# Optimization experiments

Hardware: AMD Instinct MI355X
Metric: run time of the kernel (lower is better)

Reference implementation:

```python
import jax, jax.numpy as jnp
import numpy as np

N = 50000   # nodes
E = 800000  # edges (avg degree 16)
IN = 128    # in_dim
R = 4       # rank
CMB = 64    # combine_dim
H = 4       # heads
D = 64      # hidden_dim per head
NEG_SLOPE = 0.2


def setup_inputs() -> dict:
    key = jax.random.key(0)
    ks = iter(jax.random.split(key, 24))
    def rnd(shape, s):
        return jax.random.normal(next(ks), shape, jnp.float32) * s
    src = jax.random.randint(next(ks), (E,), 0, N, jnp.int32)
    dst = jax.random.randint(next(ks), (E,), 0, N, jnp.int32)
    ones = jnp.ones((N, 1), jnp.float32)
    # buffers built in __init__: features with a trailing ones column
    h_common = jnp.concatenate([rnd((N, IN), 1.0), ones], axis=-1)      # (N, 129)
    h_type = jnp.concatenate([rnd((N, 512), 1.0), ones], axis=-1)       # (N, 513)
    h_rel = jnp.concatenate([rnd((N, 512), 1.0), ones], axis=-1)        # (N, 513)
    return {
        'src': src, 'dst': dst,
        'h_common': h_common, 'h_type': h_type, 'h_rel': h_rel,
        'Wc': rnd((R, IN + 1, CMB), 0.05),
        'Wt': rnd((R, 513, CMB), 0.05),
        'Wr': rnd((R, 513, CMB), 0.05),
        'fw': rnd((1, R), 0.5),
        'fb': rnd((1, CMB), 0.1),
        'W0': rnd((CMB, H * D), 0.05),
        'al0': rnd((H, D), 0.05), 'ar0': rnd((H, D), 0.05),
        'b0': rnd((H * D,), 0.05),
        'W1': rnd((H * D, H * D), 0.05),
        'al1': rnd((H, D), 0.05), 'ar1': rnd((H, D), 0.05),
        'b1': rnd((H * D,), 0.05),
    }


def _gat_layer(h, src, dst, W, al, ar, b, residual):
    # h: (N, F_in) -> out: (N, H*D), attention a: (E, H)
    feat = (h @ W).reshape(N, H, D)
    el = jnp.einsum('nhd,hd->nh', feat, al)  # (N, H)
    er = jnp.einsum('nhd,hd->nh', feat, ar)
    e = jax.nn.leaky_relu(el[src] + er[dst], NEG_SLOPE)  # (E, H)
    # edge softmax over incoming edges of each dst node
    m = jax.ops.segment_max(e, dst, num_segments=N)      # (N, H)
    ee = jnp.exp(e - m[dst])
    s = jax.ops.segment_sum(ee, dst, num_segments=N)
    a = ee / s[dst]                                       # (E, H)
    msg = feat[src] * a[:, :, None]                       # (E, H, D)
    out = jax.ops.segment_sum(msg, dst, num_segments=N)   # (N, H, D)
    if residual:
        out = out + h.reshape(N, H, D)
    out = out + b.reshape(1, H, D)
    return out.reshape(N, H * D), a


def reference(src, dst, h_common, h_type, h_rel, Wc, Wt, Wr, fw, fb,
              W0, al0, ar0, b0, W1, al1, ar1, b1):
    # low-rank trilinear fusion
    fc = jnp.einsum('ni,ric->rnc', h_common, Wc)  # (R, N, CMB)
    ft = jnp.einsum('ni,ric->rnc', h_type, Wt)
    fr = jnp.einsum('ni,ric->rnc', h_rel, Wr)
    zy = fc * ft * fr
    h = jnp.einsum('r,rnc->nc', fw[0], zy) + fb   # (N, CMB)
    h = jax.nn.elu(h)
    # stacked GAT layers
    h, att = _gat_layer(h, src, dst, W0, al0, ar0, b0, residual=False)
    h, att = _gat_layer(h, src, dst, W1, al1, ar1, b1, residual=True)
    return h, att
```

## Files before the change

### kernel.cpp

```cpp
#include <hip/hip_runtime.h>
#include <math.h>

#define NN 50000
#define EE 800000
#define NEG 0.2f
#define NG (NN / 16)

using f32x4  = __attribute__((ext_vector_type(4))) float;
using bf16x8 = __attribute__((ext_vector_type(8))) short;

__device__ __forceinline__ float lrelu(float x){ return x > 0.f ? x : NEG*x; }

__device__ __forceinline__ unsigned short f2b(float f){
    unsigned int u = __float_as_uint(f);
    return (unsigned short)((u + 0x7FFFu + ((u >> 16) & 1u)) >> 16);
}
__device__ __forceinline__ float b2f(unsigned short h){
    return __uint_as_float(((unsigned int)h) << 16);
}
__device__ __forceinline__ void gld_lds16(const void* g, void* l){
    __builtin_amdgcn_global_load_lds(
        (const __attribute__((address_space(1))) unsigned int*)g,
        (__attribute__((address_space(3))) unsigned int*)l, 16, 0, 0);
}

__global__ void pack_w_fusion(const float* __restrict__ W, unsigned short* __restrict__ out,
                              int K, int NKC)
{
    int u = blockIdx.x * blockDim.x + threadIdx.x;
    if (u >= NKC * 16 * 64) return;
    int l = u & 63, chunk = (u >> 6) & 15, kc = u >> 10;
    int ct = chunk >> 2, r = chunk & 3;
    int c = ct * 16 + (l & 15);
    int kb = kc * 32 + (l >> 4) * 8;
    bf16x8 v;
#pragma unroll
    for (int j = 0; j < 8; ++j)
        v[j] = (short)f2b(W[((size_t)r * K + kb + j) * 64 + c]);
    *(bf16x8*)(out + (size_t)u * 8) = v;
}

template<int PERM>
__global__ void pack_w_gemm(const float* __restrict__ W, unsigned short* __restrict__ out,
                            int K, int C)
{
    int NCH = C / 16;
    int total = (K / 32) * NCH * 64;
    int u = blockIdx.x * blockDim.x + threadIdx.x;
    if (u >= total) return;
    int l = u & 63, ch = (u >> 6) % NCH, kc = u / (64 * NCH);
    int c = ch * 16 + (l & 15);
    int kb = kc * 32 + (l >> 4) * 8;
    bf16x8 v;
#pragma unroll
    for (int j = 0; j < 8; ++j) {
        int k = kb + j;
        int ko = PERM ? ((k & 3) * 64 + (k >> 2)) : k;
        v[j] = (short)f2b(W[(size_t)ko * C + c]);
    }
    *(bf16x8*)(out + (size_t)u * 8) = v;
}

template<int KT, int NKC>
__global__ __launch_bounds__(256) void pack_a_tile(
    const float* __restrict__ F, unsigned short* __restrict__ out)
{
    constexpr int TILES = NKC / 4;
    __shared__ float sf[16][130];
    const int tid = threadIdx.x;
    const int g = blockIdx.x / TILES, t = blockIdx.x % TILES;
    const int nb = g * 16, k0 = t * 128;

#pragma unroll
    for (int i = 0; i < 8; ++i) {
        int idx = tid + i * 256;
        int row = idx >> 7, k = idx & 127;
        sf[row][k] = F[(size_t)(nb + row) * KT + k0 + k];
    }
    __syncthreads();
    {
        int kcl = tid >> 6, l = tid & 63;
        int row = l & 15, kb = kcl * 32 + (l >> 4) * 8;
        bf16x8 o;
#pragma unroll
        for (int j = 0; j < 8; ++j) o[j] = (short)f2b(sf[row][kb + j]);
        *(bf16x8*)(out + ((size_t)(g * NKC + t * 4 + kcl) * 64 + l) * 8) = o;
    }
}

template<int NKC>
__device__ __forceinline__ void fusion_pass_lds(
    const unsigned short* __restrict__ ldsA, int cbase,
    const unsigned short* __restrict__ wp,
    const float* __restrict__ W, int K, int w, int l, f32x4 (&acc)[4])
{
    const int c_lo = l & 15;
#pragma unroll
    for (int ct = 0; ct < 4; ++ct) {
        float wi = W[((size_t)w * K + (K - 1)) * 64 + ct * 16 + c_lo];
        acc[ct] = f32x4{wi, wi, wi, wi};
    }
#pragma unroll
    for (int kc = 0; kc < NKC; ++kc) {
        bf16x8 af = *(const bf16x8*)(ldsA + (cbase + kc) * 512 + l * 8);
        const unsigned short* wk = wp + (size_t)kc * 8192 + w * 512 + l * 8;
#pragma unroll
        for (int ct = 0; ct < 4; ++ct) {
            bf16x8 bf = *(const bf16x8*)(wk + ct * 2048);
            acc[ct] = __builtin_amdgcn_mfma_f32_16x16x32_bf16(af, bf, acc[ct], 0, 0, 0);
        }
    }
}

__global__ __launch_bounds__(256) void fusion_mfma(
    const unsigned short* __restrict__ apc, const unsigned short* __restrict__ apt,
    const unsigned short* __restrict__ apr,
    const unsigned short* __restrict__ wpc, const unsigned short* __restrict__ wpt,
    const unsigned short* __restrict__ wpr,
    const float* __restrict__ Wc, const float* __restrict__ Wt, const float* __restrict__ Wr,
    const float* __restrict__ fw, const float* __restrict__ fb,
    unsigned short* __restrict__ h0b)
{
    __shared__ __align__(16) char smem[36864];
    unsigned short* ldsA = (unsigned short*)smem;
    float* ldsx = (float*)smem;
    const int w = threadIdx.x >> 6, l = threadIdx.x & 63;
    const int G = blockIdx.x;

#pragma unroll
    for (int j = 0; j < 9; ++j) {
        int cid = w * 9 + j;
        const unsigned short* s;
        if (cid < 4)       s = apc + ((size_t)G * 4  + cid) * 512;
        else if (cid < 20) s = apt + ((size_t)G * 16 + (cid - 4)) * 512;
        else               s = apr + ((size_t)G * 16 + (cid - 20)) * 512;
        gld_lds16(s + l * 8, ldsA + cid * 512);
    }
    __syncthreads();

    f32x4 prod[4], acc[4];
    fusion_pass_lds<4>(ldsA, 0, wpc, Wc, 129, w, l, acc);
#pragma unroll
    for (int ct = 0; ct < 4; ++ct) prod[ct] = acc[ct];
    fusion_pass_lds<16>(ldsA, 4, wpt, Wt, 513, w, l, acc);
#pragma unroll
    for (int ct = 0; ct < 4; ++ct) prod[ct] *= acc[ct];
    fusion_pass_lds<16>(ldsA, 20, wpr, Wr, 513, w, l, acc);
    const float fww = fw[w];
#pragma unroll
    for (int ct = 0; ct < 4; ++ct) prod[ct] = prod[ct] * acc[ct] * fww;

    __syncthreads();
#pragma unroll
    for (int ct = 0; ct < 4; ++ct)
        *(f32x4*)&ldsx[((w * 4 + ct) * 64 + l) * 4] = prod[ct];
    __syncthreads();

    f32x4 s = *(const f32x4*)&ldsx[((0 * 4 + w) * 64 + l) * 4];
#pragma unroll
    for (int r = 1; r < 4; ++r)
        s += *(const f32x4*)&ldsx[((r * 4 + w) * 64 + l) * 4];

    const int c = w * 16 + (l & 15);
    const float fbc = fb[c];
#pragma unroll
    for (int q = 0; q < 4; ++q) {
        int n = G * 16 + (l >> 4) * 4 + q;
        float v = s[q] + fbc;
        v = v > 0.f ? v : expm1f(v);
        h0b[(size_t)n * 64 + c] = f2b(v);
    }
}

template<int K>
__global__ __launch_bounds__(256) void gemm_reg(
    const unsigned short* __restrict__ Ab, const unsigned short* __restrict__ wp,
    const float* __restrict__ al, const float* __restrict__ ar,
    unsigned short* __restrict__ featb,
    float* __restrict__ el, float* __restrict__ er)
{
    constexpr int NKC = K / 32;
    const int w = threadIdx.x >> 6, l = threadIdx.x & 63;
    const int nb = blockIdx.x * 16;

    f32x4 acc[4];
#pragma unroll
    for (int i = 0; i < 4; ++i) acc[i] = f32x4{0.f, 0.f, 0.f, 0.f};

    const unsigned short* abase = Ab + (size_t)(nb + (l & 15)) * K + (l >> 4) * 8;
    bf16x8 afs[NKC];
#pragma unroll
    for (int kc = 0; kc < NKC; ++kc)
        afs[kc] = *(const bf16x8*)(abase + kc * 32);

    bf16x8 bcur[4];
    {
        const unsigned short* wk = wp + (size_t)(0 * 16 + w * 4) * 512 + l * 8;
#pragma unroll
        for (int i = 0; i < 4; ++i) bcur[i] = *(const bf16x8*)(wk + i * 512);
    }
#pragma unroll
    for (int kc = 0; kc < NKC; ++kc) {
        bf16x8 bnxt[4];
        if (kc + 1 < NKC) {
            const unsigned short* wk = wp + ((size_t)(kc + 1) * 16 + w * 4) * 512 + l * 8;
#pragma unroll
            for (int i = 0; i < 4; ++i) bnxt[i] = *(const bf16x8*)(wk + i * 512);
        }
#pragma unroll
        for (int i = 0; i < 4; ++i)
            acc[i] = __builtin_amdgcn_mfma_f32_16x16x32_bf16(afs[kc], bcur[i], acc[i], 0, 0, 0);
        if (kc + 1 < NKC) {
#pragma unroll
            for (int i = 0; i < 4; ++i) bcur[i] = bnxt[i];
        }
    }

#pragma unroll
    for (int i = 0; i < 4; ++i) {
        int c = (w * 4 + i) * 16 + (l & 15);
        int dm = (c & 63) * 4 + (c >> 6);
#pragma unroll
        for (int q = 0; q < 4; ++q) {
            int n = nb + (l >> 4) * 4 + q;
            featb[(size_t)n * 256 + dm] = f2b(acc[i][q]);
        }
    }

    float pel[4] = {0.f, 0.f, 0.f, 0.f};
    float per_[4] = {0.f, 0.f, 0.f, 0.f};
#pragma unroll
    for (int i = 0; i < 4; ++i) {
        int d = i * 16 + (l & 15);
        float av = al[w * 64 + d];
        float rv = ar[w * 64 + d];
#pragma unroll
        for (int q = 0; q < 4; ++q) {
            pel[q] += acc[i][q] * av;
            per_[q] += acc[i][q] * rv;
        }
    }
#pragma unroll
    for (int off = 1; off <= 8; off <<= 1) {
#pragma unroll
        for (int q = 0; q < 4; ++q) {
            pel[q] += __shfl_xor(pel[q], off);
            per_[q] += __shfl_xor(per_[q], off);
        }
    }
    int qsel = l & 15;
    if (qsel < 4) {
        float ev = qsel == 0 ? pel[0] : qsel == 1 ? pel[1] : qsel == 2 ? pel[2] : pel[3];
        float rv = qsel == 0 ? per_[0] : qsel == 1 ? per_[1] : qsel == 2 ? per_[2] : per_[3];
        int n = nb + (l >> 4) * 4 + qsel;
        el[(size_t)n * 4 + w] = ev;
        er[(size_t)n * 4 + w] = rv;
    }
}

__global__ void hist_kernel(const int* __restrict__ dst, int* __restrict__ cnt)
{
    int e = blockIdx.x * blockDim.x + threadIdx.x;
    if (e < EE) atomicAdd(&cnt[dst[e]], 1);
}

__global__ __launch_bounds__(1024) void scan_kernel(const int* __restrict__ cnt, int* __restrict__ offs)
{
    __shared__ int tmp[1024];
    const int t = threadIdx.x;
    const int C = (NN + 1023) / 1024;
    int lo = t * C, hi = min(lo + C, NN);
    int s = 0;
    for (int i = lo; i < hi; ++i) s += cnt[i];
    tmp[t] = s;
    __syncthreads();
    for (int off = 1; off < 1024; off <<= 1) {
        int v = (t >= off) ? tmp[t - off] : 0;
        __syncthreads();
        tmp[t] += v;
        __syncthreads();
    }
    int run = (t == 0) ? 0 : tmp[t - 1];
    for (int i = lo; i < hi; ++i) { offs[i] = run; run += cnt[i]; }
    if (t == 1023) offs[NN] = tmp[1023];
}

__global__ void scatter_kernel(const int* __restrict__ dst, const int* __restrict__ offs,
                               int* __restrict__ cur, int* __restrict__ esort)
{
    int e = blockIdx.x * blockDim.x + threadIdx.x;
    if (e < EE) {
        int d = dst[e];
        int p = offs[d] + atomicAdd(&cur[d], 1);
        esort[p] = e;
    }
}

template <int RESID, int WATT, int WB16, int WF32>
__global__ __launch_bounds__(256) void gat_agg(
    const int* __restrict__ esort, const int* __restrict__ src, const int* __restrict__ offs,
    const unsigned short* __restrict__ featb,
    const float* __restrict__ el, const float* __restrict__ er,
    const unsigned short* __restrict__ residb, const float* __restrict__ bias,
    float* __restrict__ out, unsigned short* __restrict__ outb,
    float4* __restrict__ att)
{
    int n = (int)((blockIdx.x * (size_t)blockDim.x + threadIdx.x) >> 6);
    int lane = threadIdx.x & 63;
    if (n >= NN) return;
    const int s0 = offs[n], s1 = offs[n + 1], deg = s1 - s0;
    const float4 r4 = *(const float4*)(er + (size_t)n * 4);

    float a0 = 0.f, a1 = 0.f, a2 = 0.f, a3 = 0.f;
    float i0, i1, i2, i3;

    if (deg <= 64) {
        int p = s0 + lane;
        bool valid = p < s1;
        int e = valid ? esort[p] : 0;
        int sv = valid ? src[e] : 0;
        float v0 = -1e30f, v1 = -1e30f, v2 = -1e30f, v3 = -1e30f;
        if (valid) {
            float4 l4 = *(const float4*)(el + (size_t)sv * 4);
            v0 = lrelu(l4.x + r4.x); v1 = lrelu(l4.y + r4.y);
            v2 = lrelu(l4.z + r4.z); v3 = lrelu(l4.w + r4.w);
        }
        float m0 = v0, m1 = v1, m2 = v2, m3 = v3;
#pragma unroll
        for (int off = 32; off; off >>= 1) {
            m0 = fmaxf(m0, __shfl_xor(m0, off));
            m1 = fmaxf(m1, __shfl_xor(m1, off));
            m2 = fmaxf(m2, __shfl_xor(m2, off));
            m3 = fmaxf(m3, __shfl_xor(m3, off));
        }
        float e0 = valid ? expf(v0 - m0) : 0.f;
        float e1 = valid ? expf(v1 - m1) : 0.f;
        float e2 = valid ? expf(v2 - m2) : 0.f;
        float e3 = valid ? expf(v3 - m3) : 0.f;
        float z0 = e0, z1 = e1, z2 = e2, z3 = e3;
#pragma unroll
        for (int off = 32; off; off >>= 1) {
            z0 += __shfl_xor(z0, off);
            z1 += __shfl_xor(z1, off);
            z2 += __shfl_xor(z2, off);
            z3 += __shfl_xor(z3, off);
        }
        float j0 = z0 > 0.f ? 1.f / z0 : 0.f;
        float j1 = z1 > 0.f ? 1.f / z1 : 0.f;
        float j2 = z2 > 0.f ? 1.f / z2 : 0.f;
        float j3 = z3 > 0.f ? 1.f / z3 : 0.f;
        e0 *= j0; e1 *= j1; e2 *= j2; e3 *= j3;
        if (WATT && valid)
            att[e] = make_float4(e0, e1, e2, e3);
        for (int jj = 0; jj < deg; ++jj) {
            float w0 = __shfl(e0, jj), w1 = __shfl(e1, jj);
            float w2 = __shfl(e2, jj), w3 = __shfl(e3, jj);
            int s = __shfl(sv, jj);
            ushort4 f = *(const ushort4*)(featb + (size_t)s * 256 + lane * 4);
            a0 += w0 * b2f(f.x);
            a1 += w1 * b2f(f.y);
            a2 += w2 * b2f(f.z);
            a3 += w3 * b2f(f.w);
        }
        i0 = i1 = i2 = i3 = 1.f;
    } else {
        float m0 = -1e30f, m1 = -1e30f, m2 = -1e30f, m3 = -1e30f;
        for (int p = s0 + lane; p < s1; p += 64) {
            int s = src[esort[p]];
            float4 l4 = *(const float4*)(el + (size_t)s * 4);
            m0 = fmaxf(m0, lrelu(l4.x + r4.x));
            m1 = fmaxf(m1, lrelu(l4.y + r4.y));
            m2 = fmaxf(m2, lrelu(l4.z + r4.z));
            m3 = fmaxf(m3, lrelu(l4.w + r4.w));
        }
#pragma unroll
        for (int off = 32; off; off >>= 1) {
            m0 = fmaxf(m0, __shfl_xor(m0, off));
            m1 = fmaxf(m1, __shfl_xor(m1, off));
            m2 = fmaxf(m2, __shfl_xor(m2, off));
            m3 = fmaxf(m3, __shfl_xor(m3, off));
        }
        float z0 = 0.f, z1 = 0.f, z2 = 0.f, z3 = 0.f;
        for (int p = s0 + lane; p < s1; p += 64) {
            int s = src[esort[p]];
            float4 l4 = *(const float4*)(el + (size_t)s * 4);
            z0 += expf(lrelu(l4.x + r4.x) - m0);
            z1 += expf(lrelu(l4.y + r4.y) - m1);
            z2 += expf(lrelu(l4.z + r4.z) - m2);
            z3 += expf(lrelu(l4.w + r4.w) - m3);
        }
#pragma unroll
        for (int off = 32; off; off >>= 1) {
            z0 += __shfl_xor(z0, off);
            z1 += __shfl_xor(z1, off);
            z2 += __shfl_xor(z2, off);
            z3 += __shfl_xor(z3, off);
        }
        i0 = z0 > 0.f ? 1.f / z0 : 0.f;
        i1 = z1 > 0.f ? 1.f / z1 : 0.f;
        i2 = z2 > 0.f ? 1.f / z2 : 0.f;
        i3 = z3 > 0.f ? 1.f / z3 : 0.f;
        for (int p = s0; p < s1; ++p) {
            int e = esort[p];
            int s = src[e];
            float4 l4 = *(const float4*)(el + (size_t)s * 4);
            float w0 = expf(lrelu(l4.x + r4.x) - m0);
            float w1 = expf(lrelu(l4.y + r4.y) - m1);
            float w2 = expf(lrelu(l4.z + r4.z) - m2);
            float w3 = expf(lrelu(l4.w + r4.w) - m3);
            ushort4 f = *(const ushort4*)(featb + (size_t)s * 256 + lane * 4);
            a0 += w0 * b2f(f.x);
            a1 += w1 * b2f(f.y);
            a2 += w2 * b2f(f.z);
            a3 += w3 * b2f(f.w);
            if (WATT && lane == 0)
                att[e] = make_float4(w0 * i0, w1 * i1, w2 * i2, w3 * i3);
        }
    }

    float o0 = a0 * i0 + bias[lane];
    float o1 = a1 * i1 + bias[64 + lane];
    float o2 = a2 * i2 + bias[128 + lane];
    float o3 = a3 * i3 + bias[192 + lane];
    if (RESID) {
        ushort4 rp = *(const ushort4*)(residb + (size_t)n * 256 + lane * 4);
        o0 += b2f(rp.x); o1 += b2f(rp.y); o2 += b2f(rp.z); o3 += b2f(rp.w);
    }
    if (WF32) {
        float* op = out + (size_t)n * 256;
        op[lane] = o0;
        op[64 + lane] = o1;
        op[128 + lane] = o2;
        op[192 + lane] = o3;
    }
    if (WB16) {
        ushort4 ob;
        ob.x = f2b(o0); ob.y = f2b(o1); ob.z = f2b(o2); ob.w = f2b(o3);
        *(ushort4*)(outb + (size_t)n * 256 + lane * 4) = ob;
    }
}

extern "C" void kernel_launch(void* const* d_in, const int* in_sizes, int n_in,
                              void* d_out, int out_size, void* d_ws, size_t ws_size,
                              hipStream_t stream)
{
    const int*   src = (const int*)d_in[0];
    const int*   dst = (const int*)d_in[1];
    const float* hc  = (const float*)d_in[2];
    const float* ht  = (const float*)d_in[3];
    const float* hr  = (const float*)d_in[4];
    const float* Wc  = (const float*)d_in[5];
    const float* Wt  = (const float*)d_in[6];
    const float* Wr  = (const float*)d_in[7];
    const float* fw  = (const float*)d_in[8];
    const float* fb  = (const float*)d_in[9];
    const float* W0  = (const float*)d_in[10];
    const float* al0 = (const float*)d_in[11];
    const float* ar0 = (const float*)d_in[12];
    const float* b0  = (const float*)d_in[13];
    const float* W1  = (const float*)d_in[14];
    const float* al1 = (const float*)d_in[15];
    const float* ar1 = (const float*)d_in[16];
    const float* b1  = (const float*)d_in[17];

    char* ws = (char*)d_ws;
    unsigned short* h0b   = (unsigned short*)(ws);
    unsigned short* h1b   = (unsigned short*)(ws + 6400000);
    unsigned short* featb = (unsigned short*)(ws + 32000000);
    float* el    = (float*)(ws + 57600000);
    float* er    = (float*)(ws + 58400000);
    int*   cnt   = (int*)  (ws + 59200000);
    int*   offs  = (int*)  (ws + 59400000);
    int*   esort = (int*)  (ws + 59600128);
    unsigned short* wpc = (unsigned short*)(ws + 62800128);
    unsigned short* wpt = (unsigned short*)(ws + 62865664);
    unsigned short* wpr = (unsigned short*)(ws + 63127808);
    unsigned short* wp0 = (unsigned short*)(ws + 63389952);
    unsigned short* wp1 = (unsigned short*)(ws + 63422720);
    if (ws_size < 63553792ull) return;

    float* outh = (float*)d_out;
    float4* atto = (float4*)(outh + (size_t)NN * 256);

    unsigned short* apt = (unsigned short*)d_out;
    unsigned short* apc = (unsigned short*)((char*)d_out + 51200000);
    unsigned short* apr = (unsigned short*)(ws + 6400000);

    pack_w_fusion<<<(4 * 16 * 64 + 255) / 256, 256, 0, stream>>>(Wc, wpc, 129, 4);
    pack_w_fusion<<<(16 * 16 * 64 + 255) / 256, 256, 0, stream>>>(Wt, wpt, 513, 16);
    pack_w_fusion<<<(16 * 16 * 64 + 255) / 256, 256, 0, stream>>>(Wr, wpr, 513, 16);
    pack_w_gemm<0><<<(2 * 16 * 64 + 255) / 256, 256, 0, stream>>>(W0, wp0, 64, 256);
    pack_w_gemm<1><<<(8 * 16 * 64 + 255) / 256, 256, 0, stream>>>(W1, wp1, 256, 256);

    pack_a_tile<129, 4><<<NG * 1, 256, 0, stream>>>(hc, apc);
    pack_a_tile<513, 16><<<NG * 4, 256, 0, stream>>>(ht, apt);
    pack_a_tile<513, 16><<<NG * 4, 256, 0, stream>>>(hr, apr);

    fusion_mfma<<<NG, 256, 0, stream>>>(apc, apt, apr, wpc, wpt, wpr,
                                        Wc, Wt, Wr, fw, fb, h0b);

    hipMemsetAsync(cnt, 0, NN * sizeof(int), stream);
    hist_kernel<<<(EE + 255) / 256, 256, 0, stream>>>(dst, cnt);
    scan_kernel<<<1, 1024, 0, stream>>>(cnt, offs);
    hipMemsetAsync(cnt, 0, NN * sizeof(int), stream);
    scatter_kernel<<<(EE + 255) / 256, 256, 0, stream>>>(dst, offs, cnt, esort);

    gemm_reg<64><<<NG, 256, 0, stream>>>(h0b, wp0, al0, ar0, featb, el, er);
    gat_agg<0, 0, 1, 0><<<(NN * 64 + 255) / 256, 256, 0, stream>>>(
        esort, src, offs, featb, el, er, nullptr, b0, nullptr, h1b, nullptr);

    gemm_reg<256><<<NG, 256, 0, stream>>>(h1b, wp1, al1, ar1, featb, el, er);
    gat_agg<1, 1, 0, 1><<<(NN * 64 + 255) / 256, 256, 0, stream>>>(
        esort, src, offs, featb, el, er, h1b, b1, outh, nullptr, atto);
}
```

Measured before the change: 548.9 us.

## Fuse activation packing into fusion GEMM via direct fp32 LDS staging

Drops the separate pack_a_tile kernels that converted the fp32 feature matrices into bf16 MFMA tiles through a global round trip. The fusion kernel now stages raw fp32 rows into LDS with 4-byte global_load_lds in two halves and converts to bf16 on read with v_cvt_pk_bf16_f32. The five weight-packing kernels are merged into one launch, and scan_kernel now clears the counts itself so the second memset can go. In exchange the loads are narrower and there is an extra LDS sync phase inside the fusion kernel.

```diff
diff --git a/kernel.cpp b/kernel.cpp
--- a/kernel.cpp
+++ b/kernel.cpp
@@ -5,6 +5,7 @@
 #define EE 800000
 #define NEG 0.2f
 #define NG (NN / 16)
+#define CHDW 576
 
 using f32x4  = __attribute__((ext_vector_type(4))) float;
 using bf16x8 = __attribute__((ext_vector_type(8))) short;
@@ -18,17 +19,20 @@
 __device__ __forceinline__ float b2f(unsigned short h){
     return __uint_as_float(((unsigned int)h) << 16);
 }
-__device__ __forceinline__ void gld_lds16(const void* g, void* l){
+__device__ __forceinline__ void gld_lds4(const void* g, void* l){
     __builtin_amdgcn_global_load_lds(
         (const __attribute__((address_space(1))) unsigned int*)g,
-        (__attribute__((address_space(3))) unsigned int*)l, 16, 0, 0);
-}
-
-__global__ void pack_w_fusion(const float* __restrict__ W, unsigned short* __restrict__ out,
-                              int K, int NKC)
-{
-    int u = blockIdx.x * blockDim.x + threadIdx.x;
-    if (u >= NKC * 16 * 64) return;
+        (__attribute__((address_space(3))) unsigned int*)l, 4, 0, 0);
+}
+__device__ __forceinline__ unsigned int cvtpk(float lo, float hi){
+    unsigned int r;
+    asm volatile("v_cvt_pk_bf16_f32 %0, %1, %2" : "=v"(r) : "v"(lo), "v"(hi));
+    return r;
+}
+
+__device__ __forceinline__ void pw_fusion_body(
+    const float* __restrict__ W, unsigned short* __restrict__ out, int K, int u)
+{
     int l = u & 63, chunk = (u >> 6) & 15, kc = u >> 10;
     int ct = chunk >> 2, r = chunk & 3;
     int c = ct * 16 + (l & 15);
@@ -40,14 +44,11 @@
     *(bf16x8*)(out + (size_t)u * 8) = v;
 }
 
-template<int PERM>
-__global__ void pack_w_gemm(const float* __restrict__ W, unsigned short* __restrict__ out,
-                            int K, int C)
+__device__ __forceinline__ void pw_gemm_body(
+    const float* __restrict__ W, unsigned short* __restrict__ out,
+    int C, int PERM, int u)
 {
     int NCH = C / 16;
-    int total = (K / 32) * NCH * 64;
-    int u = blockIdx.x * blockDim.x + threadIdx.x;
-    if (u >= total) return;
     int l = u & 63, ch = (u >> 6) % NCH, kc = u / (64 * NCH);
     int c = ch * 16 + (l & 15);
     int kb = kc * 32 + (l >> 4) * 8;
@@ -61,91 +62,138 @@
     *(bf16x8*)(out + (size_t)u * 8) = v;
 }
 
-template<int KT, int NKC>
-__global__ __launch_bounds__(256) void pack_a_tile(
-    const float* __restrict__ F, unsigned short* __restrict__ out)
-{
-    constexpr int TILES = NKC / 4;
-    __shared__ float sf[16][130];
-    const int tid = threadIdx.x;
-    const int g = blockIdx.x / TILES, t = blockIdx.x % TILES;
-    const int nb = g * 16, k0 = t * 128;
-
-#pragma unroll
-    for (int i = 0; i < 8; ++i) {
-        int idx = tid + i * 256;
-        int row = idx >> 7, k = idx & 127;
-        sf[row][k] = F[(size_t)(nb + row) * KT + k0 + k];
-    }
-    __syncthreads();
-    {
-        int kcl = tid >> 6, l = tid & 63;
-        int row = l & 15, kb = kcl * 32 + (l >> 4) * 8;
-        bf16x8 o;
-#pragma unroll
-        for (int j = 0; j < 8; ++j) o[j] = (short)f2b(sf[row][kb + j]);
-        *(bf16x8*)(out + ((size_t)(g * NKC + t * 4 + kcl) * 64 + l) * 8) = o;
-    }
-}
-
-template<int NKC>
-__device__ __forceinline__ void fusion_pass_lds(
-    const unsigned short* __restrict__ ldsA, int cbase,
-    const unsigned short* __restrict__ wp,
-    const float* __restrict__ W, int K, int w, int l, f32x4 (&acc)[4])
-{
-    const int c_lo = l & 15;
-#pragma unroll
-    for (int ct = 0; ct < 4; ++ct) {
-        float wi = W[((size_t)w * K + (K - 1)) * 64 + ct * 16 + c_lo];
-        acc[ct] = f32x4{wi, wi, wi, wi};
-    }
-#pragma unroll
-    for (int kc = 0; kc < NKC; ++kc) {
-        bf16x8 af = *(const bf16x8*)(ldsA + (cbase + kc) * 512 + l * 8);
-        const unsigned short* wk = wp + (size_t)kc * 8192 + w * 512 + l * 8;
-#pragma unroll
-        for (int ct = 0; ct < 4; ++ct) {
-            bf16x8 bf = *(const bf16x8*)(wk + ct * 2048);
-            acc[ct] = __builtin_amdgcn_mfma_f32_16x16x32_bf16(af, bf, acc[ct], 0, 0, 0);
-        }
-    }
+__global__ __launch_bounds__(256) void pack_all_w(
+    const float* __restrict__ Wc, const float* __restrict__ Wt, const float* __restrict__ Wr,
+    const float* __restrict__ W0, const float* __restrict__ W1,
+    unsigned short* __restrict__ wpc, unsigned short* __restrict__ wpt,
+    unsigned short* __restrict__ wpr, unsigned short* __restrict__ wp0,
+    unsigned short* __restrict__ wp1)
+{
+    int b = blockIdx.x, t = threadIdx.x;
+    if (b < 16)        pw_fusion_body(Wc, wpc, 129, b * 256 + t);
+    else if (b < 80)   pw_fusion_body(Wt, wpt, 513, (b - 16) * 256 + t);
+    else if (b < 144)  pw_fusion_body(Wr, wpr, 513, (b - 80) * 256 + t);
+    else if (b < 152)  pw_gemm_body(W0, wp0, 256, 0, (b - 144) * 256 + t);
+    else               pw_gemm_body(W1, wp1, 256, 1, (b - 152) * 256 + t);
 }
 
 __global__ __launch_bounds__(256) void fusion_mfma(
-    const unsigned short* __restrict__ apc, const unsigned short* __restrict__ apt,
-    const unsigned short* __restrict__ apr,
+    const float* __restrict__ hc, const float* __restrict__ ht, const float* __restrict__ hr,
     const unsigned short* __restrict__ wpc, const unsigned short* __restrict__ wpt,
     const unsigned short* __restrict__ wpr,
     const float* __restrict__ Wc, const float* __restrict__ Wt, const float* __restrict__ Wr,
     const float* __restrict__ fw, const float* __restrict__ fb,
     unsigned short* __restrict__ h0b)
 {
-    __shared__ __align__(16) char smem[36864];
-    unsigned short* ldsA = (unsigned short*)smem;
-    float* ldsx = (float*)smem;
+    __shared__ __align__(16) float lds[18 * CHDW];
+    float* ldsx = lds;
     const int w = threadIdx.x >> 6, l = threadIdx.x & 63;
-    const int G = blockIdx.x;
-
-#pragma unroll
-    for (int j = 0; j < 9; ++j) {
-        int cid = w * 9 + j;
-        const unsigned short* s;
-        if (cid < 4)       s = apc + ((size_t)G * 4  + cid) * 512;
-        else if (cid < 20) s = apt + ((size_t)G * 16 + (cid - 4)) * 512;
-        else               s = apr + ((size_t)G * 16 + (cid - 20)) * 512;
-        gld_lds16(s + l * 8, ldsA + cid * 512);
-    }
+    const int G = blockIdx.x, nb = G * 16;
+    const int c_lo = l & 15;
+
+    int rowi[9], koffi[9];
+#pragma unroll
+    for (int i = 0; i < 9; ++i) {
+        int u = i * 64 + l;
+        rowi[i] = u / 36;
+        int off = u - rowi[i] * 36;
+        koffi[i] = off > 31 ? 31 : off;
+    }
+
+    const int abase_l = (l & 15) * 36 + (l >> 4) * 8;
+    auto aread = [&](int slot) -> bf16x8 {
+        const float* p = lds + slot * CHDW + abase_l;
+        f32x4 a = *(const f32x4*)p;
+        f32x4 b = *(const f32x4*)(p + 4);
+        union { unsigned int wd[4]; bf16x8 v; } u;
+        u.wd[0] = cvtpk(a[0], a[1]);
+        u.wd[1] = cvtpk(a[2], a[3]);
+        u.wd[2] = cvtpk(b[0], b[1]);
+        u.wd[3] = cvtpk(b[2], b[3]);
+        return u.v;
+    };
+
+    auto stage_half = [&](int half) {
+        for (int cid = w; cid < 18; cid += 4) {
+            int gcid = half * 18 + cid;
+            const float* F; int K, kc;
+            if (gcid < 4)       { F = hc; K = 129; kc = gcid; }
+            else if (gcid < 20) { F = ht; K = 513; kc = gcid - 4; }
+            else                { F = hr; K = 513; kc = gcid - 20; }
+#pragma unroll
+            for (int i = 0; i < 9; ++i) {
+                const float* g = F + (size_t)(nb + rowi[i]) * K + kc * 32 + koffi[i];
+                gld_lds4(g, (char*)(lds + cid * CHDW + i * 64));
+            }
+        }
+    };
+
+    f32x4 prod[4], accT[4], acc[4];
+
+    stage_half(0);
     __syncthreads();
 
-    f32x4 prod[4], acc[4];
-    fusion_pass_lds<4>(ldsA, 0, wpc, Wc, 129, w, l, acc);
-#pragma unroll
-    for (int ct = 0; ct < 4; ++ct) prod[ct] = acc[ct];
-    fusion_pass_lds<16>(ldsA, 4, wpt, Wt, 513, w, l, acc);
-#pragma unroll
-    for (int ct = 0; ct < 4; ++ct) prod[ct] *= acc[ct];
-    fusion_pass_lds<16>(ldsA, 20, wpr, Wr, 513, w, l, acc);
+#pragma unroll
+    for (int ct = 0; ct < 4; ++ct) {
+        float wi = Wc[((size_t)w * 129 + 128) * 64 + ct * 16 + c_lo];
+        prod[ct] = f32x4{wi, wi, wi, wi};
+    }
+#pragma unroll
+    for (int kc = 0; kc < 4; ++kc) {
+        bf16x8 af = aread(kc);
+        const unsigned short* wk = wpc + (size_t)kc * 8192 + w * 512 + l * 8;
+#pragma unroll
+        for (int ct = 0; ct < 4; ++ct) {
+            bf16x8 bf = *(const bf16x8*)(wk + ct * 2048);
+            prod[ct] = __builtin_amdgcn_mfma_f32_16x16x32_bf16(af, bf, prod[ct], 0, 0, 0);
+        }
+    }
+#pragma unroll
+    for (int ct = 0; ct < 4; ++ct) {
+        float wi = Wt[((size_t)w * 513 + 512) * 64 + ct * 16 + c_lo];
+        accT[ct] = f32x4{wi, wi, wi, wi};
+    }
+#pragma unroll
+    for (int kc = 0; kc < 14; ++kc) {
+        bf16x8 af = aread(4 + kc);
+        const unsigned short* wk = wpt + (size_t)kc * 8192 + w * 512 + l * 8;
+#pragma unroll
+        for (int ct = 0; ct < 4; ++ct) {
+            bf16x8 bf = *(const bf16x8*)(wk + ct * 2048);
+            accT[ct] = __builtin_amdgcn_mfma_f32_16x16x32_bf16(af, bf, accT[ct], 0, 0, 0);
+        }
+    }
+
+    __syncthreads();
+    stage_half(1);
+    __syncthreads();
+
+#pragma unroll
+    for (int kc = 14; kc < 16; ++kc) {
+        bf16x8 af = aread(kc - 14);
+        const unsigned short* wk = wpt + (size_t)kc * 8192 + w * 512 + l * 8;
+#pragma unroll
+        for (int ct = 0; ct < 4; ++ct) {
+            bf16x8 bf = *(const bf16x8*)(wk + ct * 2048);
+            accT[ct] = __builtin_amdgcn_mfma_f32_16x16x32_bf16(af, bf, accT[ct], 0, 0, 0);
+        }
+    }
+#pragma unroll
+    for (int ct = 0; ct < 4; ++ct) {
+        prod[ct] *= accT[ct];
+        float wi = Wr[((size_t)w * 513 + 512) * 64 + ct * 16 + c_lo];
+        acc[ct] = f32x4{wi, wi, wi, wi};
+    }
+#pragma unroll
+    for (int kc = 0; kc < 16; ++kc) {
+        bf16x8 af = aread(2 + kc);
+        const unsigned short* wk = wpr + (size_t)kc * 8192 + w * 512 + l * 8;
+#pragma unroll
+        for (int ct = 0; ct < 4; ++ct) {
+            bf16x8 bf = *(const bf16x8*)(wk + ct * 2048);
+            acc[ct] = __builtin_amdgcn_mfma_f32_16x16x32_bf16(af, bf, acc[ct], 0, 0, 0);
+        }
+    }
     const float fww = fw[w];
 #pragma unroll
     for (int ct = 0; ct < 4; ++ct) prod[ct] = prod[ct] * acc[ct] * fww;
@@ -161,11 +209,11 @@
     for (int r = 1; r < 4; ++r)
         s += *(const f32x4*)&ldsx[((r * 4 + w) * 64 + l) * 4];
 
-    const int c = w * 16 + (l & 15);
+    const int c = w * 16 + c_lo;
     const float fbc = fb[c];
 #pragma unroll
     for (int q = 0; q < 4; ++q) {
-        int n = G * 16 + (l >> 4) * 4 + q;
+        int n = nb + (l >> 4) * 4 + q;
         float v = s[q] + fbc;
         v = v > 0.f ? v : expm1f(v);
         h0b[(size_t)n * 64 + c] = f2b(v);
@@ -264,7 +312,7 @@
     if (e < EE) atomicAdd(&cnt[dst[e]], 1);
 }
 
-__global__ __launch_bounds__(1024) void scan_kernel(const int* __restrict__ cnt, int* __restrict__ offs)
+__global__ __launch_bounds__(1024) void scan_kernel(int* __restrict__ cnt, int* __restrict__ offs)
 {
     __shared__ int tmp[1024];
     const int t = threadIdx.x;
@@ -281,7 +329,7 @@
         __syncthreads();
     }
     int run = (t == 0) ? 0 : tmp[t - 1];
-    for (int i = lo; i < hi; ++i) { offs[i] = run; run += cnt[i]; }
+    for (int i = lo; i < hi; ++i) { offs[i] = run; run += cnt[i]; cnt[i] = 0; }
     if (t == 1023) offs[NN] = tmp[1023];
 }
 
@@ -482,27 +530,14 @@
     float* outh = (float*)d_out;
     float4* atto = (float4*)(outh + (size_t)NN * 256);
 
-    unsigned short* apt = (unsigned short*)d_out;
-    unsigned short* apc = (unsigned short*)((char*)d_out + 51200000);
-    unsigned short* apr = (unsigned short*)(ws + 6400000);
-
-    pack_w_fusion<<<(4 * 16 * 64 + 255) / 256, 256, 0, stream>>>(Wc, wpc, 129, 4);
-    pack_w_fusion<<<(16 * 16 * 64 + 255) / 256, 256, 0, stream>>>(Wt, wpt, 513, 16);
-    pack_w_fusion<<<(16 * 16 * 64 + 255) / 256, 256, 0, stream>>>(Wr, wpr, 513, 16);
-    pack_w_gemm<0><<<(2 * 16 * 64 + 255) / 256, 256, 0, stream>>>(W0, wp0, 64, 256);
-    pack_w_gemm<1><<<(8 * 16 * 64 + 255) / 256, 256, 0, stream>>>(W1, wp1, 256, 256);
-
-    pack_a_tile<129, 4><<<NG * 1, 256, 0, stream>>>(hc, apc);
-    pack_a_tile<513, 16><<<NG * 4, 256, 0, stream>>>(ht, apt);
-    pack_a_tile<513, 16><<<NG * 4, 256, 0, stream>>>(hr, apr);
-
-    fusion_mfma<<<NG, 256, 0, stream>>>(apc, apt, apr, wpc, wpt, wpr,
+    pack_all_w<<<184, 256, 0, stream>>>(Wc, Wt, Wr, W0, W1, wpc, wpt, wpr, wp0, wp1);
+
+    fusion_mfma<<<NG, 256, 0, stream>>>(hc, ht, hr, wpc, wpt, wpr,
                                         Wc, Wt, Wr, fw, fb, h0b);
 
     hipMemsetAsync(cnt, 0, NN * sizeof(int), stream);
     hist_kernel<<<(EE + 255) / 256, 256, 0, stream>>>(dst, cnt);
     scan_kernel<<<1, 1024, 0, stream>>>(cnt, offs);
-    hipMemsetAsync(cnt, 0, NN * sizeof(int), stream);
     scatter_kernel<<<(EE + 255) / 256, 256, 0, stream>>>(dst, offs, cnt, esort);
 
     gemm_reg<64><<<NG, 256, 0, stream>>>(h0b, wp0, al0, ar0, featb, el, er);
```

New measurement: 531.5 us. -3.2%, faster.
